# Kernel tuning notes

Hardware: AMD Instinct MI355X
Metric: run time of the kernel (lower is better)

## Reference

```python
import jax, jax.numpy as jnp
import numpy as np

N, L, C, DEM = 32, 2048, 256, 8


def setup_inputs() -> dict:
    key = jax.random.key(0)
    ks = jax.random.split(key, 4)
    return {
        "dem": jax.random.normal(ks[0], (N, DEM), jnp.float32),
        "x": jax.random.normal(ks[1], (N, L, C), jnp.float32),
        # 3 LayerNorm normalizers (max/avg/sum), stacked on leading axis
        "ln_gamma": jnp.ones((3, C), jnp.float32),
        "ln_beta": jnp.zeros((3, C), jnp.float32),
        # dem_fc: Linear(8,40) -> ReLU -> Linear(40,20) -> ReLU
        "w1": jax.random.normal(ks[2], (DEM, 40), jnp.float32) * 0.1,
        "b1": jnp.zeros((40,), jnp.float32),
        "w2": jax.random.normal(ks[3], (40, 20), jnp.float32) * 0.1,
        "b2": jnp.zeros((20,), jnp.float32),
    }


def _layernorm(x, g, b, eps=1e-5):
    mu = x.mean(-1, keepdims=True)
    var = x.var(-1, keepdims=True)  # biased, matches torch LayerNorm
    return (x - mu) / jnp.sqrt(var + eps) * g + b


def _cummax_with_idx(x):
    """Causal running max + argmax index along axis 1. x: (N, L, C)."""
    xT = jnp.moveaxis(x, 1, 0)  # (L, N, C)
    ts = jnp.arange(x.shape[1], dtype=jnp.int32)

    def step(carry, inp):
        m, mi = carry
        xt, t = inp
        take = xt > m
        nm = jnp.where(take, xt, m)
        ni = jnp.where(take, t, mi)
        return (nm, ni), (nm, ni)

    init = (jnp.full((x.shape[0], x.shape[2]), -jnp.inf, x.dtype),
            jnp.zeros((x.shape[0], x.shape[2]), jnp.int32))
    _, (cm, ci) = jax.lax.scan(step, init, (xT, ts))
    return jnp.moveaxis(cm, 0, 1), jnp.moveaxis(ci, 0, 1)


def reference(dem, x, ln_gamma, ln_beta, w1, b1, w2, b2):
    Nn, Ll, Cc = x.shape
    # O(L) scan equivalent of zero-padded max_pool1d(kernel=L, stride=1).
    cm, ci = _cummax_with_idx(x)
    pad_mask = (jnp.arange(Ll) < Ll - 1)[None, :, None]
    pad_wins = pad_mask & (cm < 0)
    p_max = jnp.where(pad_wins, jnp.zeros((), x.dtype), cm)
    p_max_ind = jnp.where(pad_wins, -1, ci)  # ind - (L-1) convention: negative -> padding

    cs = jnp.cumsum(x, axis=1)
    p_avg = cs / jnp.asarray(Ll, x.dtype)            # avg_pool1d with kernel=L (zeros counted)
    p_sum = cs / jnp.sqrt(jnp.asarray(Ll, x.dtype))  # norm_sum_pool1d: sum / sqrt(kernel)

    pm = _layernorm(p_max, ln_gamma[0], ln_beta[0])
    pa = _layernorm(p_avg, ln_gamma[1], ln_beta[1])
    ps = _layernorm(p_sum, ln_gamma[2], ln_beta[2])

    d = jax.nn.relu(jax.nn.relu(dem @ w1 + b1) @ w2 + b2)  # (N, 20)
    d = jnp.broadcast_to(d[:, None, :], (Nn, Ll, d.shape[-1]))

    out = jnp.concatenate([pm, pa, ps, d], axis=-1)  # (N, L, 3C + 20)
    return out, p_max_ind, jax.lax.stop_gradient(p_max)
```

## Files before the change

kernel.cpp:

```cpp
#include <hip/hip_runtime.h>
#include <math.h>

typedef float f4 __attribute__((ext_vector_type(4)));
typedef int   i4 __attribute__((ext_vector_type(4)));

#define Nn     32
#define Ll     2048
#define Cc     256
#define DEMd   8
#define H1d    40
#define H2d    20
#define OUTC   (3 * Cc + H2d)
#define CHUNKS 128
#define CLEN   (Ll / CHUNKS)
#define CPT    4
#define TPB    (Cc / CPT)

#define DPP_ADD(x, ctrl, rm)                                                   \
    x += __builtin_bit_cast(float, __builtin_amdgcn_update_dpp(                \
             0, __builtin_bit_cast(int, x), ctrl, rm, 0xf, false))

__device__ __forceinline__ float wave_sum(float x)
{
    DPP_ADD(x, 0x111, 0xf);
    DPP_ADD(x, 0x112, 0xf);
    DPP_ADD(x, 0x114, 0xf);
    DPP_ADD(x, 0x118, 0xf);
    DPP_ADD(x, 0x142, 0xa);
    DPP_ADD(x, 0x143, 0xc);
    return __builtin_bit_cast(float,
        __builtin_amdgcn_readlane(__builtin_bit_cast(int, x), 63));
}

__global__ __launch_bounds__(TPB) void chunk_agg_kernel(
    const float* __restrict__ x,
    float* __restrict__ aggM, int* __restrict__ aggI, float* __restrict__ aggS)
{
    const int bid = blockIdx.x;
    const int n  = bid / CHUNKS;
    const int ch = bid % CHUNKS;
    const int c4 = threadIdx.x * CPT;

    const float* xp = x + ((size_t)(n * Ll + ch * CLEN)) * Cc + c4;

    f4 m = {-INFINITY, -INFINITY, -INFINITY, -INFINITY};
    i4 mi = {0, 0, 0, 0};
    f4 s = {0.f, 0.f, 0.f, 0.f};

    #pragma unroll
    for (int tl = 0; tl < CLEN; ++tl) {
        const f4 v = *reinterpret_cast<const f4*>(xp + (size_t)tl * Cc);
        const int t = ch * CLEN + tl;
        #pragma unroll
        for (int k = 0; k < CPT; ++k) {
            if (v[k] > m[k]) { m[k] = v[k]; mi[k] = t; }
            s[k] += v[k];
        }
    }
    const int o = (n * CHUNKS + ch) * Cc + c4;
    *reinterpret_cast<f4*>(aggM + o) = m;
    *reinterpret_cast<i4*>(aggI + o) = mi;
    *reinterpret_cast<f4*>(aggS + o) = s;
}

__global__ __launch_bounds__(TPB) void prefix_kernel(
    float* __restrict__ aggM, int* __restrict__ aggI, float* __restrict__ aggS)
{
    const int idx = blockIdx.x * TPB + threadIdx.x;
    const int n = idx >> 8;
    const int c = idx & (Cc - 1);

    float m = -INFINITY; int mi = 0; float s = 0.f;
    #pragma unroll 4
    for (int j = 0; j < CHUNKS; ++j) {
        const int o = (n * CHUNKS + j) * Cc + c;
        const float am = aggM[o];
        const int   ai = aggI[o];
        const float as = aggS[o];
        aggM[o] = m; aggI[o] = mi; aggS[o] = s;
        if (am > m) { m = am; mi = ai; }
        s += as;
    }
}

__global__ __launch_bounds__(TPB) void pool_ln_kernel(
    const float* __restrict__ x,
    const float* __restrict__ dem,
    const float* __restrict__ lng, const float* __restrict__ lnb,
    const float* __restrict__ w1, const float* __restrict__ b1,
    const float* __restrict__ w2, const float* __restrict__ b2,
    const float* __restrict__ aggM, const int* __restrict__ aggI,
    const float* __restrict__ aggS,
    float* __restrict__ o1, float* __restrict__ o2, float* __restrict__ o3)
{
    __shared__ float h1s[H1d];
    __shared__ __align__(16) float dvec[H2d];

    const int bid  = blockIdx.x;
    const int n    = bid / CHUNKS;
    const int ch   = bid % CHUNKS;
    const int lane = threadIdx.x;
    const int c4   = lane * CPT;

    if (lane < H1d) {
        float a = b1[lane];
        #pragma unroll
        for (int k = 0; k < DEMd; ++k) a += dem[n * DEMd + k] * w1[k * H1d + lane];
        h1s[lane] = fmaxf(a, 0.f);
    }
    __syncthreads();
    if (lane < H2d) {
        float a = b2[lane];
        #pragma unroll
        for (int k = 0; k < H1d; ++k) a += h1s[k] * w2[k * H2d + lane];
        dvec[lane] = fmaxf(a, 0.f);
    }
    __syncthreads();
    f4 dvf = {0.f, 0.f, 0.f, 0.f};
    if (lane < H2d / CPT) dvf = *reinterpret_cast<const f4*>(dvec + lane * CPT);

    const int co = (n * CHUNKS + ch) * Cc + c4;
    f4 m  = *reinterpret_cast<const f4*>(aggM + co);
    i4 mi = *reinterpret_cast<const i4*>(aggI + co);
    f4 s  = *reinterpret_cast<const f4*>(aggS + co);

    const f4 g0 = *reinterpret_cast<const f4*>(lng + c4);
    const f4 g1 = *reinterpret_cast<const f4*>(lng + Cc + c4);
    const f4 g2 = *reinterpret_cast<const f4*>(lng + 2 * Cc + c4);
    const f4 be0 = *reinterpret_cast<const f4*>(lnb + c4);
    const f4 be1 = *reinterpret_cast<const f4*>(lnb + Cc + c4);
    const f4 be2 = *reinterpret_cast<const f4*>(lnb + 2 * Cc + c4);

    const float invC  = 1.0f / (float)Cc;
    const float invL  = 1.0f / (float)Ll;
    const float invSL = 0.022097086912079612f;

    const float* xp = x + ((size_t)(n * Ll + ch * CLEN)) * Cc + c4;

    f4 v = *reinterpret_cast<const f4*>(xp);

    for (int tl = 0; tl < CLEN; ++tl) {
        const int t = ch * CLEN + tl;

        f4 vn;
        if (tl + 1 < CLEN)
            vn = *reinterpret_cast<const f4*>(xp + (size_t)(tl + 1) * Cc);

        f4 pm; f4 pidxf;
        float s0 = 0.f, s2 = 0.f;
        const bool notlast = (t < Ll - 1);
        #pragma unroll
        for (int k = 0; k < CPT; ++k) {
            if (v[k] > m[k]) { m[k] = v[k]; mi[k] = t; }
            s[k] += v[k];
            const bool pad = notlast && (m[k] < 0.f);
            const float p  = pad ? 0.f : m[k];
            pm[k]    = p;
            pidxf[k] = pad ? -1.0f : (float)mi[k];
            s0 += p;
            s2 += s[k];
        }

        const float muM = wave_sum(s0) * invC;
        const float csm = wave_sum(s2) * invC;

        float s1 = 0.f, s3 = 0.f;
        f4 dcs;
        #pragma unroll
        for (int k = 0; k < CPT; ++k) {
            const float dm = pm[k] - muM;
            dcs[k] = s[k] - csm;
            s1 += dm * dm;
            s3 += dcs[k] * dcs[k];
        }
        const float varM  = wave_sum(s1) * invC;
        const float varCS = wave_sum(s3) * invC;

        const float rM = rsqrtf(varM + 1e-5f);
        const float rA = invL  * rsqrtf(varCS * invL * invL + 1e-5f);
        const float rS = invSL * rsqrtf(varCS * invL + 1e-5f);

        f4 y0, y1, y2;
        #pragma unroll
        for (int k = 0; k < CPT; ++k) {
            y0[k] = (pm[k] - muM) * rM * g0[k] + be0[k];
            y1[k] = dcs[k] * rA * g1[k] + be1[k];
            y2[k] = dcs[k] * rS * g2[k] + be2[k];
        }

        const size_t row = (size_t)(n * Ll + t);
        float* orow = o1 + row * OUTC;
        __builtin_nontemporal_store(y0, reinterpret_cast<f4*>(orow + c4));
        __builtin_nontemporal_store(y1, reinterpret_cast<f4*>(orow + Cc + c4));
        __builtin_nontemporal_store(y2, reinterpret_cast<f4*>(orow + 2 * Cc + c4));
        if (lane < H2d / CPT)
            __builtin_nontemporal_store(dvf, reinterpret_cast<f4*>(orow + 3 * Cc + lane * CPT));
        __builtin_nontemporal_store(pidxf, reinterpret_cast<f4*>(o2 + row * Cc + c4));
        __builtin_nontemporal_store(pm,    reinterpret_cast<f4*>(o3 + row * Cc + c4));

        v = vn;
    }
}

extern "C" void kernel_launch(void* const* d_in, const int* in_sizes, int n_in,
                              void* d_out, int out_size, void* d_ws, size_t ws_size,
                              hipStream_t stream)
{
    const float* dem = (const float*)d_in[0];
    const float* x   = (const float*)d_in[1];
    const float* lng = (const float*)d_in[2];
    const float* lnb = (const float*)d_in[3];
    const float* w1  = (const float*)d_in[4];
    const float* b1  = (const float*)d_in[5];
    const float* w2  = (const float*)d_in[6];
    const float* b2  = (const float*)d_in[7];

    float* out = (float*)d_out;
    float* o1 = out;
    float* o2 = o1 + (size_t)Nn * Ll * OUTC;
    float* o3 = o2 + (size_t)Nn * Ll * Cc;

    const size_t nAgg = (size_t)Nn * CHUNKS * Cc;
    float* aggM = (float*)d_ws;
    int*   aggI = (int*)(aggM + nAgg);
    float* aggS = (float*)(aggI + nAgg);

    chunk_agg_kernel<<<dim3(Nn * CHUNKS), dim3(TPB), 0, stream>>>(x, aggM, aggI, aggS);
    prefix_kernel<<<dim3((Nn * Cc) / TPB), dim3(TPB), 0, stream>>>(aggM, aggI, aggS);
    pool_ln_kernel<<<dim3(Nn * CHUNKS), dim3(TPB), 0, stream>>>(
        x, dem, lng, lnb, w1, b1, w2, b2, aggM, aggI, aggS, o1, o2, o3);
}
```

Baseline: 433.0 us.

## Drop separate prefix kernel; each block folds preceding chunk aggregates itself

Removes the serial prefix-scan kernel over chunk aggregates. Each pool/LN block now reduces the aggregates of all earlier chunks in its own prologue, so one launch and the sequential 128-step scan with its global read/write round trip go away. The chunk count is halved to 64, which doubles rows per block and keeps the redundant prefix work per block shorter. The cost is redundant reads of aggregates (quadratic in chunks), fewer blocks, and a longer serial loop per block that may leave the GPU underfilled.

```diff
diff --git a/kernel.cpp b/kernel.cpp
--- a/kernel.cpp
+++ b/kernel.cpp
@@ -11,7 +11,7 @@
 #define H1d    40
 #define H2d    20
 #define OUTC   (3 * Cc + H2d)
-#define CHUNKS 128
+#define CHUNKS 64
 #define CLEN   (Ll / CHUNKS)
 #define CPT    4
 #define TPB    (Cc / CPT)
@@ -47,7 +47,7 @@
     i4 mi = {0, 0, 0, 0};
     f4 s = {0.f, 0.f, 0.f, 0.f};
 
-    #pragma unroll
+    #pragma unroll 4
     for (int tl = 0; tl < CLEN; ++tl) {
         const f4 v = *reinterpret_cast<const f4*>(xp + (size_t)tl * Cc);
         const int t = ch * CLEN + tl;
@@ -61,26 +61,6 @@
     *reinterpret_cast<f4*>(aggM + o) = m;
     *reinterpret_cast<i4*>(aggI + o) = mi;
     *reinterpret_cast<f4*>(aggS + o) = s;
-}
-
-__global__ __launch_bounds__(TPB) void prefix_kernel(
-    float* __restrict__ aggM, int* __restrict__ aggI, float* __restrict__ aggS)
-{
-    const int idx = blockIdx.x * TPB + threadIdx.x;
-    const int n = idx >> 8;
-    const int c = idx & (Cc - 1);
-
-    float m = -INFINITY; int mi = 0; float s = 0.f;
-    #pragma unroll 4
-    for (int j = 0; j < CHUNKS; ++j) {
-        const int o = (n * CHUNKS + j) * Cc + c;
-        const float am = aggM[o];
-        const int   ai = aggI[o];
-        const float as = aggS[o];
-        aggM[o] = m; aggI[o] = mi; aggS[o] = s;
-        if (am > m) { m = am; mi = ai; }
-        s += as;
-    }
 }
 
 __global__ __launch_bounds__(TPB) void pool_ln_kernel(
@@ -119,10 +99,24 @@
     f4 dvf = {0.f, 0.f, 0.f, 0.f};
     if (lane < H2d / CPT) dvf = *reinterpret_cast<const f4*>(dvec + lane * CPT);
 
-    const int co = (n * CHUNKS + ch) * Cc + c4;
-    f4 m  = *reinterpret_cast<const f4*>(aggM + co);
-    i4 mi = *reinterpret_cast<const i4*>(aggI + co);
-    f4 s  = *reinterpret_cast<const f4*>(aggS + co);
+    f4 m = {-INFINITY, -INFINITY, -INFINITY, -INFINITY};
+    i4 mi = {0, 0, 0, 0};
+    f4 s = {0.f, 0.f, 0.f, 0.f};
+    {
+        const float* pM = aggM + (size_t)(n * CHUNKS) * Cc + c4;
+        const int*   pI = aggI + (size_t)(n * CHUNKS) * Cc + c4;
+        const float* pS = aggS + (size_t)(n * CHUNKS) * Cc + c4;
+        for (int j = 0; j < ch; ++j) {
+            const f4 am = *reinterpret_cast<const f4*>(pM + (size_t)j * Cc);
+            const i4 ai = *reinterpret_cast<const i4*>(pI + (size_t)j * Cc);
+            const f4 as = *reinterpret_cast<const f4*>(pS + (size_t)j * Cc);
+            #pragma unroll
+            for (int k = 0; k < CPT; ++k) {
+                if (am[k] > m[k]) { m[k] = am[k]; mi[k] = ai[k]; }
+                s[k] += as[k];
+            }
+        }
+    }
 
     const f4 g0 = *reinterpret_cast<const f4*>(lng + c4);
     const f4 g1 = *reinterpret_cast<const f4*>(lng + Cc + c4);
@@ -226,7 +220,6 @@
     float* aggS = (float*)(aggI + nAgg);
 
     chunk_agg_kernel<<<dim3(Nn * CHUNKS), dim3(TPB), 0, stream>>>(x, aggM, aggI, aggS);
-    prefix_kernel<<<dim3((Nn * Cc) / TPB), dim3(TPB), 0, stream>>>(aggM, aggI, aggS);
     pool_ln_kernel<<<dim3(Nn * CHUNKS), dim3(TPB), 0, stream>>>(
         x, dem, lng, lnb, w1, b1, w2, b2, aggM, aggI, aggS, o1, o2, o3);
 }
```

After: 424.6 us. About the same (-1.9%).
